# Kernel tuning notes

Measured on AMD Instinct MI355X. Metric: run time of the kernel, lower is better.

Reference implementation:

```python
import jax, jax.numpy as jnp
import numpy as np

F_FEAT = 310   # len(feature_names)
B = 2048       # samples; x has F_FEAT*B elements
H = 32         # sfp_neurons


def _uniform(key, shape, bound):
    return jax.random.uniform(key, shape, jnp.float32, -bound, bound)


def setup_inputs() -> dict:
    key = jax.random.key(0)
    ks = jax.random.split(key, 7)
    x = jax.random.normal(ks[0], (F_FEAT, B), dtype=jnp.float32)
    # Stacked per-feature MLP params (torch Linear default init: U(-1/sqrt(fan_in), +)).
    s1 = 1.0 / np.sqrt(F_FEAT - 1)
    s2 = 1.0 / np.sqrt(H)
    W1 = _uniform(ks[1], (F_FEAT, F_FEAT - 1, H), s1)  # (in, out) layout
    b1 = _uniform(ks[2], (F_FEAT, H), s1)
    W2 = _uniform(ks[3], (F_FEAT, H, H), s2)
    b2 = _uniform(ks[4], (F_FEAT, H), s2)
    W3 = _uniform(ks[5], (F_FEAT, H, H), s2)
    b3 = _uniform(ks[6], (F_FEAT, H), s2)
    return {"x": x, "W1": W1, "b1": b1, "W2": W2, "b2": b2, "W3": W3, "b3": b3}


def reference(x, W1, b1, W2, b2, W3, b3):
    F_, B_ = x.shape
    # Leave-one-out gather: for SFP i, rows [0..i-1, i+1..F-1] of x (feature-major),
    # then the original's view(-1, 1, F-1) reinterprets the flat buffer as (B, F-1).
    idx = jnp.arange(F_ - 1)[None, :]
    idx = idx + (idx >= jnp.arange(F_)[:, None])          # (F, F-1)
    X = x[idx].reshape(F_, B_, F_ - 1)                    # (F, B, F-1) grouped inputs
    h = jax.nn.relu(jnp.einsum('fbk,fkh->fbh', X, W1) + b1[:, None, :])
    h = jax.nn.relu(jnp.einsum('fbh,fhg->fbg', h, W2) + b2[:, None, :])
    h = jax.nn.relu(jnp.einsum('fbh,fhg->fbg', h, W3) + b3[:, None, :])  # (F, B, H)
    # torch.cat of per-SFP .view(-1) == row-major flatten of (F, B, H)
    return h.reshape(-1)
```

## Files before the change

kernel.cpp:

```cpp
#include <hip/hip_runtime.h>

namespace {

constexpr int F_FEAT = 310;
constexpr int KDIM   = 309;
constexpr int BSZ    = 2048;
constexpr int HDIM   = 32;
constexpr int NCH    = 10;
constexpr int NX     = F_FEAT * BSZ;

constexpr int    NBLK8    = NX / 8 + 2;
constexpr size_t CSTR_B   = (size_t)NBLK8 * 16;
constexpr size_t XC_BYTES = CSTR_B * 8;
constexpr size_t W1T_FSTR = 32 * 320 * 2;
constexpr size_t W1T_OFF  = XC_BYTES;
constexpr size_t W2T_OFF  = W1T_OFF + (size_t)F_FEAT * W1T_FSTR;
constexpr size_t WT_FSTR  = 32 * 32 * 2;
constexpr size_t W3T_OFF  = W2T_OFF + (size_t)F_FEAT * WT_FSTR;
constexpr size_t WS_NEED  = W3T_OFF + (size_t)F_FEAT * WT_FSTR;

constexpr int NBX      = (NBLK8 + 255) / 256;
constexpr int CVT_XBLK = NBX * 8;
constexpr int CVT_BLK  = CVT_XBLK + F_FEAT * 6;

typedef __bf16 bf16x8 __attribute__((ext_vector_type(8)));
typedef float  f32x4  __attribute__((ext_vector_type(4)));
typedef int    i32x4  __attribute__((ext_vector_type(4)));

#define MFMA(a, b, c) __builtin_amdgcn_mfma_f32_16x16x32_bf16((a), (b), (c), 0, 0, 0)

__global__ __launch_bounds__(256) void cvt_all(
    const float* __restrict__ x,  const float* __restrict__ W1,
    const float* __restrict__ W2, const float* __restrict__ W3,
    char* __restrict__ ws)
{
    __shared__ float tile[64][33];
    const int b = blockIdx.x, tid = threadIdx.x;

    if (b < CVT_XBLK) {
        const int c = b / NBX, mb = b - c * NBX;
        const int m = mb * 256 + tid;
        if (m >= NBLK8) return;
        const int e0 = m * 8 - c;
        bf16x8 v;
        #pragma unroll
        for (int q = 0; q < 8; ++q) {
            const int i = e0 + q;
            v[q] = (__bf16)((i >= 0 && i < NX) ? x[i] : 0.f);
        }
        *(bf16x8*)(ws + (size_t)c * CSTR_B + (size_t)m * 16) = v;
        return;
    }

    const int wb = b - CVT_XBLK;
    const int fi = wb / 6, part = wb - fi * 6;

    if (part < 5) {
        const float* Wg = W1 + (size_t)fi * KDIM * HDIM;
        const int row = tid >> 2;
        const int c8  = (tid & 3) * 8;
        const int k   = part * 64 + row;
        float4 f0 = make_float4(0,0,0,0), f1 = f0;
        if (k < KDIM) {
            f0 = *(const float4*)&Wg[k * HDIM + c8];
            f1 = *(const float4*)&Wg[k * HDIM + c8 + 4];
        }
        tile[row][c8+0] = f0.x; tile[row][c8+1] = f0.y;
        tile[row][c8+2] = f0.z; tile[row][c8+3] = f0.w;
        tile[row][c8+4] = f1.x; tile[row][c8+5] = f1.y;
        tile[row][c8+6] = f1.z; tile[row][c8+7] = f1.w;
        __syncthreads();
        const int h = tid & 31, kq = (tid >> 5) * 8;
        bf16x8 o;
        #pragma unroll
        for (int j = 0; j < 8; ++j) o[j] = (__bf16)tile[kq + j][h];
        const int boff = (h * 640 + part * 128 + kq * 2) ^ ((h & 7) << 4);
        *(bf16x8*)(ws + W1T_OFF + (size_t)fi * W1T_FSTR + (size_t)boff) = o;
    } else {
        const int kl = tid >> 3, h4 = (tid & 7) * 4;
        const int h = tid & 31, kq = (tid >> 5) * 8;
        {
            const float* Wg = W2 + (size_t)fi * HDIM * HDIM;
            float4 f = *(const float4*)&Wg[kl * HDIM + h4];
            tile[kl][h4+0] = f.x; tile[kl][h4+1] = f.y;
            tile[kl][h4+2] = f.z; tile[kl][h4+3] = f.w;
            __syncthreads();
            if (tid < 128) {
                bf16x8 o;
                #pragma unroll
                for (int j = 0; j < 8; ++j) o[j] = (__bf16)tile[kq + j][h];
                *(bf16x8*)(ws + W2T_OFF + (size_t)fi * WT_FSTR + (size_t)(h * 32 + kq) * 2) = o;
            }
            __syncthreads();
        }
        {
            const float* Wg = W3 + (size_t)fi * HDIM * HDIM;
            float4 f = *(const float4*)&Wg[kl * HDIM + h4];
            tile[kl][h4+0] = f.x; tile[kl][h4+1] = f.y;
            tile[kl][h4+2] = f.z; tile[kl][h4+3] = f.w;
            __syncthreads();
            if (tid < 128) {
                bf16x8 o;
                #pragma unroll
                for (int j = 0; j < 8; ++j) o[j] = (__bf16)tile[kq + j][h];
                *(bf16x8*)(ws + W3T_OFF + (size_t)fi * WT_FSTR + (size_t)(h * 32 + kq) * 2) = o;
            }
        }
    }
}

template<bool FAST>
__global__ __launch_bounds__(256, 4) void sfp6(
    const float* __restrict__ x,
    const float* __restrict__ W1, const float* __restrict__ b1,
    const float* __restrict__ W2, const float* __restrict__ b2,
    const float* __restrict__ W3, const float* __restrict__ b3,
    const char* __restrict__ ws, float* __restrict__ out)
{
    __shared__ __attribute__((aligned(16))) __bf16 W1s[32 * 320];
    __shared__ __attribute__((aligned(16))) __bf16 h1s[256 * 40];

    const int fi = blockIdx.x >> 3, sb = blockIdx.x & 7;

    const int tid = threadIdx.x, lane = tid & 63, wv = tid >> 6;
    const int l15 = lane & 15, l16 = lane >> 4;
    const int lk8 = l16 * 8, r0 = l16 * 4;
    const int b0 = sb << 8, iB = fi << 11;
    const int mrow = wv * 64;

    int d[4];
    unsigned off[4];
    #pragma unroll
    for (int m = 0; m < 4; ++m) {
        const int lin = (b0 + mrow + 16 * m + l15) * KDIM + lk8;
        d[m] = iB - lin;
        const int c8 = (-lin) & 7;
        off[m] = (unsigned)((size_t)c8 * CSTR_B) + (unsigned)(lin + c8) * 2u;
    }

    auto fragW1 = [&](int c, int hrow) -> bf16x8 {
        if (FAST) {
            const int boff = (hrow * 640 + c * 64 + l16 * 16) ^ ((hrow & 7) << 4);
            return *(const bf16x8*)((const char*)W1s + boff);
        } else {
            const float* Wg = W1 + (size_t)fi * KDIM * HDIM;
            bf16x8 r;
            #pragma unroll
            for (int q = 0; q < 8; ++q) {
                const int k = c * 32 + lk8 + q;
                r[q] = (__bf16)((k < KDIM) ? Wg[k * HDIM + hrow] : 0.f);
            }
            return r;
        }
    };

    f32x4 acc[4][2];
    #pragma unroll
    for (int m = 0; m < 4; ++m) { acc[m][0] = {0,0,0,0}; acc[m][1] = {0,0,0,0}; }

    if constexpr (FAST) {
        {
            const char* src = ws + W1T_OFF + (size_t)fi * W1T_FSTR;
            #pragma unroll
            for (int i = 0; i < 5; ++i) {
                const int o = i * 4096 + tid * 16;
                *(bf16x8*)((char*)W1s + o) = *(const bf16x8*)(src + o);
            }
        }
        __syncthreads();

        bf16x8 ab[3][4];

        auto issueLd = [&](int c) {
            #pragma unroll
            for (int m = 0; m < 4; ++m) {
                const unsigned sel = (32 * c >= d[m]) ? 4096u : 0u;
                const char* p = ws + (off[m] + (unsigned)(64 * c) + sel);
                i32x4 r;
                asm volatile("global_load_dwordx4 %0, %1, off" : "=v"(r) : "v"(p));
                ab[c % 3][m] = __builtin_bit_cast(bf16x8, r);
            }
        };

        issueLd(0);
        issueLd(1);

        #pragma unroll
        for (int c = 0; c < NCH; ++c) {
            if (c + 2 < NCH) issueLd(c + 2);
            bf16x8 w0 = fragW1(c, l15), w1 = fragW1(c, 16 + l15);
            if (c <= 7)      asm volatile("s_waitcnt vmcnt(8)");
            else if (c == 8) asm volatile("s_waitcnt vmcnt(4)");
            else             asm volatile("s_waitcnt vmcnt(0)");
            __builtin_amdgcn_sched_barrier(0);

            const bool h0 = (unsigned)(d[0] - 32*c - 1) < 7u;
            const bool h1 = (unsigned)(d[1] - 32*c - 1) < 7u;
            const bool h2 = (unsigned)(d[2] - 32*c - 1) < 7u;
            const bool h3 = (unsigned)(d[3] - 32*c - 1) < 7u;
            if (__any(h0 | h1 | h2 | h3)) {
                #pragma unroll
                for (int m = 0; m < 4; ++m) {
                    const bool hm = (unsigned)(d[m] - 32*c - 1) < 7u;
                    if (hm) {
                        const int li_ = iB - d[m] + 32*c;
                        bf16x8 r;
                        #pragma unroll
                        for (int q = 0; q < 8; ++q) {
                            int i = li_ + q; i += (i >= iB) ? BSZ : 0;
                            r[q] = *(const __bf16*)(ws + (size_t)i * 2);
                        }
                        ab[c % 3][m] = r;
                    }
                }
            }

            #pragma unroll
            for (int m = 0; m < 4; ++m) {
                acc[m][0] = MFMA(ab[c % 3][m], w0, acc[m][0]);
                acc[m][1] = MFMA(ab[c % 3][m], w1, acc[m][1]);
            }
        }
        __builtin_amdgcn_sched_barrier(0);
    } else {
        auto fragA = [&](int li_) -> bf16x8 {
            bf16x8 r;
            #pragma unroll
            for (int q = 0; q < 8; ++q) {
                int i = li_ + q; i += (i >= iB) ? BSZ : 0;
                i = (i < NX) ? i : (NX - 1);
                r[q] = (__bf16)x[i];
            }
            return r;
        };
        for (int c = 0; c < NCH; ++c) {
            bf16x8 w0 = fragW1(c, l15), w1 = fragW1(c, 16 + l15);
            #pragma unroll
            for (int m = 0; m < 4; ++m) {
                bf16x8 a = fragA(iB - d[m] + 32 * c);
                acc[m][0] = MFMA(a, w0, acc[m][0]);
                acc[m][1] = MFMA(a, w1, acc[m][1]);
            }
        }
    }

    bf16x8 w2a, w2b, w3a, w3b;
    if (FAST) {
        const char* p2 = ws + W2T_OFF + (size_t)fi * WT_FSTR;
        const char* p3 = ws + W3T_OFF + (size_t)fi * WT_FSTR;
        w2a = *(const bf16x8*)(p2 + (size_t)(l15 * 32 + lk8) * 2);
        w2b = *(const bf16x8*)(p2 + (size_t)((16 + l15) * 32 + lk8) * 2);
        w3a = *(const bf16x8*)(p3 + (size_t)(l15 * 32 + lk8) * 2);
        w3b = *(const bf16x8*)(p3 + (size_t)((16 + l15) * 32 + lk8) * 2);
    } else {
        #pragma unroll
        for (int q = 0; q < 8; ++q) {
            const size_t base2 = (size_t)fi * HDIM * HDIM + (lk8 + q) * HDIM;
            w2a[q] = (__bf16)W2[base2 + l15];      w2b[q] = (__bf16)W2[base2 + 16 + l15];
            w3a[q] = (__bf16)W3[base2 + l15];      w3b[q] = (__bf16)W3[base2 + 16 + l15];
        }
    }
    const float b1v0 = b1[fi*HDIM + l15], b1v1 = b1[fi*HDIM + 16 + l15];
    const float b2v0 = b2[fi*HDIM + l15], b2v1 = b2[fi*HDIM + 16 + l15];
    const float b3v0 = b3[fi*HDIM + l15], b3v1 = b3[fi*HDIM + 16 + l15];

    constexpr int LDA = 40;
    #pragma unroll
    for (int m = 0; m < 4; ++m)
        #pragma unroll
        for (int r = 0; r < 4; ++r) {
            float v;
            v = acc[m][0][r] + b1v0; h1s[(mrow + 16*m + r0 + r)*LDA +      l15] = (__bf16)(v > 0.f ? v : 0.f);
            v = acc[m][1][r] + b1v1; h1s[(mrow + 16*m + r0 + r)*LDA + 16 + l15] = (__bf16)(v > 0.f ? v : 0.f);
        }

    const f32x4 z = {0,0,0,0};
    f32x4 c2[4][2];
    #pragma unroll
    for (int m = 0; m < 4; ++m) {
        bf16x8 ha = *(const bf16x8*)&h1s[(mrow + 16*m + l15)*LDA + lk8];
        c2[m][0] = MFMA(ha, w2a, z);
        c2[m][1] = MFMA(ha, w2b, z);
    }
    #pragma unroll
    for (int m = 0; m < 4; ++m)
        #pragma unroll
        for (int r = 0; r < 4; ++r) {
            float v;
            v = c2[m][0][r] + b2v0; h1s[(mrow + 16*m + r0 + r)*LDA +      l15] = (__bf16)(v > 0.f ? v : 0.f);
            v = c2[m][1][r] + b2v1; h1s[(mrow + 16*m + r0 + r)*LDA + 16 + l15] = (__bf16)(v > 0.f ? v : 0.f);
        }

    const size_t orow = (size_t)(fi * BSZ + b0 + mrow);
    #pragma unroll
    for (int m = 0; m < 4; ++m) {
        bf16x8 ha = *(const bf16x8*)&h1s[(mrow + 16*m + l15)*LDA + lk8];
        f32x4 c30 = MFMA(ha, w3a, z);
        f32x4 c31 = MFMA(ha, w3b, z);
        #pragma unroll
        for (int r = 0; r < 4; ++r) {
            float v;
            v = c30[r] + b3v0; out[(orow + 16*m + r0 + r)*HDIM +      l15] = v > 0.f ? v : 0.f;
            v = c31[r] + b3v1; out[(orow + 16*m + r0 + r)*HDIM + 16 + l15] = v > 0.f ? v : 0.f;
        }
    }
}

}

extern "C" void kernel_launch(void* const* d_in, const int* in_sizes, int n_in,
                              void* d_out, int out_size, void* d_ws, size_t ws_size,
                              hipStream_t stream) {
    const float* x  = (const float*)d_in[0];
    const float* W1 = (const float*)d_in[1];
    const float* b1 = (const float*)d_in[2];
    const float* W2 = (const float*)d_in[3];
    const float* b2 = (const float*)d_in[4];
    const float* W3 = (const float*)d_in[5];
    const float* b3 = (const float*)d_in[6];
    float* out = (float*)d_out;
    char* ws = (char*)d_ws;

    const bool fast = (ws != nullptr) && (ws_size >= WS_NEED);
    if (fast) {
        hipLaunchKernelGGL(cvt_all, dim3(CVT_BLK), dim3(256), 0, stream, x, W1, W2, W3, ws);
        hipLaunchKernelGGL((sfp6<true>), dim3(F_FEAT * 8), dim3(256), 0, stream,
                           x, W1, b1, W2, b2, W3, b3, ws, out);
    } else {
        hipLaunchKernelGGL((sfp6<false>), dim3(F_FEAT * 8), dim3(256), 0, stream,
                           x, W1, b1, W2, b2, W3, b3, ws, out);
    }
}
```

Baseline: 75.09 us.

## Reuse register-resident input rows across features with double-buffered W1 in LDS

Restructures the main kernel so each block owns 64 batch rows and loops over a chunk of about 20 features. The block loads its leave-one-out input fragments (both shifted variants) into registers once and reuses them for every feature, instead of reloading input per feature. The next feature's transposed W1 is prefetched into a second LDS buffer while the current one is used. The grid shrinks from 2480 to 512 blocks and the per-feature work per wave becomes small, so latency hiding and occupancy may suffer.

```diff
diff --git a/kernel.cpp b/kernel.cpp
--- a/kernel.cpp
+++ b/kernel.cpp
@@ -25,7 +25,6 @@
 
 typedef __bf16 bf16x8 __attribute__((ext_vector_type(8)));
 typedef float  f32x4  __attribute__((ext_vector_type(4)));
-typedef int    i32x4  __attribute__((ext_vector_type(4)));
 
 #define MFMA(a, b, c) __builtin_amdgcn_mfma_f32_16x16x32_bf16((a), (b), (c), 0, 0, 0)
 
@@ -109,156 +108,183 @@
     }
 }
 
-template<bool FAST>
-__global__ __launch_bounds__(256, 4) void sfp6(
+__global__ __launch_bounds__(256, 3) void sfp9(
+    const float* __restrict__ b1, const float* __restrict__ b2,
+    const float* __restrict__ b3,
+    const char* __restrict__ ws, float* __restrict__ out)
+{
+    __shared__ __attribute__((aligned(16))) __bf16 Wbuf[2][32 * 320];
+    __shared__ __attribute__((aligned(16))) __bf16 hb[4][16 * 40];
+
+    const int sb = blockIdx.x >> 4, fc = blockIdx.x & 15;
+    const int f0 = (fc * F_FEAT) >> 4, f1 = ((fc + 1) * F_FEAT) >> 4;
+    const int b0 = sb * 64;
+
+    const int tid = threadIdx.x, lane = tid & 63, wv = tid >> 6;
+    const int l15 = lane & 15, l16 = lane >> 4;
+    const int lk8 = l16 * 8, r0 = l16 * 4;
+
+    const int row  = b0 + wv * 16 + l15;
+    const int lin0 = row * KDIM + lk8;
+    const int c8   = (-lin0) & 7;
+    const char* abase = ws + (size_t)c8 * CSTR_B + (size_t)(lin0 + c8) * 2;
+
+    bf16x8 lo[NCH], hi[NCH];
+    #pragma unroll
+    for (int c = 0; c < NCH; ++c) {
+        lo[c] = *(const bf16x8*)(abase + 64 * c);
+        hi[c] = *(const bf16x8*)(abase + 64 * c + 4096);
+    }
+
+    {
+        const char* src = ws + W1T_OFF + (size_t)f0 * W1T_FSTR;
+        #pragma unroll
+        for (int i = 0; i < 5; ++i) {
+            const int o = i * 4096 + tid * 16;
+            *(bf16x8*)((char*)Wbuf[0] + o) = *(const bf16x8*)(src + o);
+        }
+    }
+    __syncthreads();
+
+    const f32x4 z = {0.f, 0.f, 0.f, 0.f};
+
+    for (int f = f0; f < f1; ++f) {
+        const int pb = (f - f0) & 1;
+
+        if (f + 1 < f1) {
+            const char* src = ws + W1T_OFF + (size_t)(f + 1) * W1T_FSTR;
+            char* dst = (char*)Wbuf[pb ^ 1];
+            #pragma unroll
+            for (int i = 0; i < 5; ++i) {
+                const int o = i * 4096 + tid * 16;
+                *(bf16x8*)(dst + o) = *(const bf16x8*)(src + o);
+            }
+        }
+
+        const char* p2 = ws + W2T_OFF + (size_t)f * WT_FSTR;
+        const char* p3 = ws + W3T_OFF + (size_t)f * WT_FSTR;
+        const bf16x8 w2a = *(const bf16x8*)(p2 + (size_t)(l15 * 32 + lk8) * 2);
+        const bf16x8 w2b = *(const bf16x8*)(p2 + (size_t)((16 + l15) * 32 + lk8) * 2);
+        const bf16x8 w3a = *(const bf16x8*)(p3 + (size_t)(l15 * 32 + lk8) * 2);
+        const bf16x8 w3b = *(const bf16x8*)(p3 + (size_t)((16 + l15) * 32 + lk8) * 2);
+        const float b1v0 = b1[f*HDIM + l15], b1v1 = b1[f*HDIM + 16 + l15];
+        const float b2v0 = b2[f*HDIM + l15], b2v1 = b2[f*HDIM + 16 + l15];
+        const float b3v0 = b3[f*HDIM + l15], b3v1 = b3[f*HDIM + 16 + l15];
+
+        const int iB = f << 11;
+        const int D  = iB - lin0;
+        const bool anyMixed =
+            __any((D > 0) & (D < 320) & ((D & 31) != 0) & ((D & 31) < 8));
+
+        f32x4 acc0 = z, acc1 = z;
+        const __bf16* Wb = Wbuf[pb];
+        #pragma unroll
+        for (int c = 0; c < NCH; ++c) {
+            const int bo0 = (l15 * 640 + c * 64 + l16 * 16) ^ ((l15 & 7) << 4);
+            const int bo1 = ((16 + l15) * 640 + c * 64 + l16 * 16) ^ (((16 + l15) & 7) << 4);
+            const bf16x8 w0 = *(const bf16x8*)((const char*)Wb + bo0);
+            const bf16x8 w1 = *(const bf16x8*)((const char*)Wb + bo1);
+            bf16x8 a;
+            if (__builtin_expect(anyMixed, 0)) {
+                #pragma unroll
+                for (int q = 0; q < 8; ++q)
+                    a[q] = (lin0 + 32 * c + q < iB) ? lo[c][q] : hi[c][q];
+            } else {
+                a = (lin0 + 32 * c + 7 < iB) ? lo[c] : hi[c];
+            }
+            acc0 = MFMA(a, w0, acc0);
+            acc1 = MFMA(a, w1, acc1);
+        }
+
+        __bf16* hw = &hb[wv][0];
+        #pragma unroll
+        for (int r = 0; r < 4; ++r) {
+            float v;
+            v = acc0[r] + b1v0; hw[(r0 + r) * 40 +      l15] = (__bf16)(v > 0.f ? v : 0.f);
+            v = acc1[r] + b1v1; hw[(r0 + r) * 40 + 16 + l15] = (__bf16)(v > 0.f ? v : 0.f);
+        }
+        {
+            const bf16x8 ha = *(const bf16x8*)&hw[l15 * 40 + lk8];
+            const f32x4 c20 = MFMA(ha, w2a, z);
+            const f32x4 c21 = MFMA(ha, w2b, z);
+            #pragma unroll
+            for (int r = 0; r < 4; ++r) {
+                float v;
+                v = c20[r] + b2v0; hw[(r0 + r) * 40 +      l15] = (__bf16)(v > 0.f ? v : 0.f);
+                v = c21[r] + b2v1; hw[(r0 + r) * 40 + 16 + l15] = (__bf16)(v > 0.f ? v : 0.f);
+            }
+        }
+        {
+            const bf16x8 h2 = *(const bf16x8*)&hw[l15 * 40 + lk8];
+            const f32x4 c30 = MFMA(h2, w3a, z);
+            const f32x4 c31 = MFMA(h2, w3b, z);
+            const size_t orow = (size_t)f * BSZ + b0 + wv * 16;
+            #pragma unroll
+            for (int r = 0; r < 4; ++r) {
+                float v;
+                v = c30[r] + b3v0; out[(orow + r0 + r)*HDIM +      l15] = v > 0.f ? v : 0.f;
+                v = c31[r] + b3v1; out[(orow + r0 + r)*HDIM + 16 + l15] = v > 0.f ? v : 0.f;
+            }
+        }
+        __syncthreads();
+    }
+}
+
+__global__ __launch_bounds__(256, 4) void sfp_fb(
     const float* __restrict__ x,
     const float* __restrict__ W1, const float* __restrict__ b1,
     const float* __restrict__ W2, const float* __restrict__ b2,
     const float* __restrict__ W3, const float* __restrict__ b3,
-    const char* __restrict__ ws, float* __restrict__ out)
+    float* __restrict__ out)
 {
-    __shared__ __attribute__((aligned(16))) __bf16 W1s[32 * 320];
     __shared__ __attribute__((aligned(16))) __bf16 h1s[256 * 40];
-
     const int fi = blockIdx.x >> 3, sb = blockIdx.x & 7;
-
     const int tid = threadIdx.x, lane = tid & 63, wv = tid >> 6;
     const int l15 = lane & 15, l16 = lane >> 4;
     const int lk8 = l16 * 8, r0 = l16 * 4;
     const int b0 = sb << 8, iB = fi << 11;
     const int mrow = wv * 64;
 
-    int d[4];
-    unsigned off[4];
-    #pragma unroll
-    for (int m = 0; m < 4; ++m) {
-        const int lin = (b0 + mrow + 16 * m + l15) * KDIM + lk8;
-        d[m] = iB - lin;
-        const int c8 = (-lin) & 7;
-        off[m] = (unsigned)((size_t)c8 * CSTR_B) + (unsigned)(lin + c8) * 2u;
-    }
-
+    auto fragA = [&](int li_) -> bf16x8 {
+        bf16x8 r;
+        #pragma unroll
+        for (int q = 0; q < 8; ++q) {
+            int i = li_ + q; i += (i >= iB) ? BSZ : 0;
+            i = (i < NX) ? i : (NX - 1);
+            r[q] = (__bf16)x[i];
+        }
+        return r;
+    };
     auto fragW1 = [&](int c, int hrow) -> bf16x8 {
-        if (FAST) {
-            const int boff = (hrow * 640 + c * 64 + l16 * 16) ^ ((hrow & 7) << 4);
-            return *(const bf16x8*)((const char*)W1s + boff);
-        } else {
-            const float* Wg = W1 + (size_t)fi * KDIM * HDIM;
-            bf16x8 r;
-            #pragma unroll
-            for (int q = 0; q < 8; ++q) {
-                const int k = c * 32 + lk8 + q;
-                r[q] = (__bf16)((k < KDIM) ? Wg[k * HDIM + hrow] : 0.f);
-            }
-            return r;
-        }
+        const float* Wg = W1 + (size_t)fi * KDIM * HDIM;
+        bf16x8 r;
+        #pragma unroll
+        for (int q = 0; q < 8; ++q) {
+            const int k = c * 32 + lk8 + q;
+            r[q] = (__bf16)((k < KDIM) ? Wg[k * HDIM + hrow] : 0.f);
+        }
+        return r;
     };
 
     f32x4 acc[4][2];
     #pragma unroll
     for (int m = 0; m < 4; ++m) { acc[m][0] = {0,0,0,0}; acc[m][1] = {0,0,0,0}; }
-
-    if constexpr (FAST) {
-        {
-            const char* src = ws + W1T_OFF + (size_t)fi * W1T_FSTR;
-            #pragma unroll
-            for (int i = 0; i < 5; ++i) {
-                const int o = i * 4096 + tid * 16;
-                *(bf16x8*)((char*)W1s + o) = *(const bf16x8*)(src + o);
-            }
-        }
-        __syncthreads();
-
-        bf16x8 ab[3][4];
-
-        auto issueLd = [&](int c) {
-            #pragma unroll
-            for (int m = 0; m < 4; ++m) {
-                const unsigned sel = (32 * c >= d[m]) ? 4096u : 0u;
-                const char* p = ws + (off[m] + (unsigned)(64 * c) + sel);
-                i32x4 r;
-                asm volatile("global_load_dwordx4 %0, %1, off" : "=v"(r) : "v"(p));
-                ab[c % 3][m] = __builtin_bit_cast(bf16x8, r);
-            }
-        };
-
-        issueLd(0);
-        issueLd(1);
-
-        #pragma unroll
-        for (int c = 0; c < NCH; ++c) {
-            if (c + 2 < NCH) issueLd(c + 2);
-            bf16x8 w0 = fragW1(c, l15), w1 = fragW1(c, 16 + l15);
-            if (c <= 7)      asm volatile("s_waitcnt vmcnt(8)");
-            else if (c == 8) asm volatile("s_waitcnt vmcnt(4)");
-            else             asm volatile("s_waitcnt vmcnt(0)");
-            __builtin_amdgcn_sched_barrier(0);
-
-            const bool h0 = (unsigned)(d[0] - 32*c - 1) < 7u;
-            const bool h1 = (unsigned)(d[1] - 32*c - 1) < 7u;
-            const bool h2 = (unsigned)(d[2] - 32*c - 1) < 7u;
-            const bool h3 = (unsigned)(d[3] - 32*c - 1) < 7u;
-            if (__any(h0 | h1 | h2 | h3)) {
-                #pragma unroll
-                for (int m = 0; m < 4; ++m) {
-                    const bool hm = (unsigned)(d[m] - 32*c - 1) < 7u;
-                    if (hm) {
-                        const int li_ = iB - d[m] + 32*c;
-                        bf16x8 r;
-                        #pragma unroll
-                        for (int q = 0; q < 8; ++q) {
-                            int i = li_ + q; i += (i >= iB) ? BSZ : 0;
-                            r[q] = *(const __bf16*)(ws + (size_t)i * 2);
-                        }
-                        ab[c % 3][m] = r;
-                    }
-                }
-            }
-
-            #pragma unroll
-            for (int m = 0; m < 4; ++m) {
-                acc[m][0] = MFMA(ab[c % 3][m], w0, acc[m][0]);
-                acc[m][1] = MFMA(ab[c % 3][m], w1, acc[m][1]);
-            }
-        }
-        __builtin_amdgcn_sched_barrier(0);
-    } else {
-        auto fragA = [&](int li_) -> bf16x8 {
-            bf16x8 r;
-            #pragma unroll
-            for (int q = 0; q < 8; ++q) {
-                int i = li_ + q; i += (i >= iB) ? BSZ : 0;
-                i = (i < NX) ? i : (NX - 1);
-                r[q] = (__bf16)x[i];
-            }
-            return r;
-        };
-        for (int c = 0; c < NCH; ++c) {
-            bf16x8 w0 = fragW1(c, l15), w1 = fragW1(c, 16 + l15);
-            #pragma unroll
-            for (int m = 0; m < 4; ++m) {
-                bf16x8 a = fragA(iB - d[m] + 32 * c);
-                acc[m][0] = MFMA(a, w0, acc[m][0]);
-                acc[m][1] = MFMA(a, w1, acc[m][1]);
-            }
+    for (int c = 0; c < NCH; ++c) {
+        bf16x8 w0 = fragW1(c, l15), w1 = fragW1(c, 16 + l15);
+        #pragma unroll
+        for (int m = 0; m < 4; ++m) {
+            bf16x8 a = fragA((b0 + mrow + 16 * m + l15) * KDIM + lk8 + 32 * c);
+            acc[m][0] = MFMA(a, w0, acc[m][0]);
+            acc[m][1] = MFMA(a, w1, acc[m][1]);
         }
     }
 
     bf16x8 w2a, w2b, w3a, w3b;
-    if (FAST) {
-        const char* p2 = ws + W2T_OFF + (size_t)fi * WT_FSTR;
-        const char* p3 = ws + W3T_OFF + (size_t)fi * WT_FSTR;
-        w2a = *(const bf16x8*)(p2 + (size_t)(l15 * 32 + lk8) * 2);
-        w2b = *(const bf16x8*)(p2 + (size_t)((16 + l15) * 32 + lk8) * 2);
-        w3a = *(const bf16x8*)(p3 + (size_t)(l15 * 32 + lk8) * 2);
-        w3b = *(const bf16x8*)(p3 + (size_t)((16 + l15) * 32 + lk8) * 2);
-    } else {
-        #pragma unroll
-        for (int q = 0; q < 8; ++q) {
-            const size_t base2 = (size_t)fi * HDIM * HDIM + (lk8 + q) * HDIM;
-            w2a[q] = (__bf16)W2[base2 + l15];      w2b[q] = (__bf16)W2[base2 + 16 + l15];
-            w3a[q] = (__bf16)W3[base2 + l15];      w3b[q] = (__bf16)W3[base2 + 16 + l15];
-        }
+    #pragma unroll
+    for (int q = 0; q < 8; ++q) {
+        const size_t base2 = (size_t)fi * HDIM * HDIM + (lk8 + q) * HDIM;
+        w2a[q] = (__bf16)W2[base2 + l15];      w2b[q] = (__bf16)W2[base2 + 16 + l15];
+        w3a[q] = (__bf16)W3[base2 + l15];      w3b[q] = (__bf16)W3[base2 + 16 + l15];
     }
     const float b1v0 = b1[fi*HDIM + l15], b1v1 = b1[fi*HDIM + 16 + l15];
     const float b2v0 = b2[fi*HDIM + l15], b2v1 = b2[fi*HDIM + 16 + l15];
@@ -273,7 +299,6 @@
             v = acc[m][0][r] + b1v0; h1s[(mrow + 16*m + r0 + r)*LDA +      l15] = (__bf16)(v > 0.f ? v : 0.f);
             v = acc[m][1][r] + b1v1; h1s[(mrow + 16*m + r0 + r)*LDA + 16 + l15] = (__bf16)(v > 0.f ? v : 0.f);
         }
-
     const f32x4 z = {0,0,0,0};
     f32x4 c2[4][2];
     #pragma unroll
@@ -290,7 +315,6 @@
             v = c2[m][0][r] + b2v0; h1s[(mrow + 16*m + r0 + r)*LDA +      l15] = (__bf16)(v > 0.f ? v : 0.f);
             v = c2[m][1][r] + b2v1; h1s[(mrow + 16*m + r0 + r)*LDA + 16 + l15] = (__bf16)(v > 0.f ? v : 0.f);
         }
-
     const size_t orow = (size_t)(fi * BSZ + b0 + mrow);
     #pragma unroll
     for (int m = 0; m < 4; ++m) {
@@ -324,10 +348,10 @@
     const bool fast = (ws != nullptr) && (ws_size >= WS_NEED);
     if (fast) {
         hipLaunchKernelGGL(cvt_all, dim3(CVT_BLK), dim3(256), 0, stream, x, W1, W2, W3, ws);
-        hipLaunchKernelGGL((sfp6<true>), dim3(F_FEAT * 8), dim3(256), 0, stream,
-                           x, W1, b1, W2, b2, W3, b3, ws, out);
+        hipLaunchKernelGGL(sfp9, dim3(32 * 16), dim3(256), 0, stream,
+                           b1, b2, b3, ws, out);
     } else {
-        hipLaunchKernelGGL((sfp6<false>), dim3(F_FEAT * 8), dim3(256), 0, stream,
-                           x, W1, b1, W2, b2, W3, b3, ws, out);
-    }
-}
+        hipLaunchKernelGGL(sfp_fb, dim3(F_FEAT * 8), dim3(256), 0, stream,
+                           x, W1, b1, W2, b2, W3, b3, out);
+    }
+}
```

Measured after the change: 71.43 us. 4.9% less time.
